# Kernel optimization log

Measured on AMD Instinct MI355X. Metric: run time of the kernel, lower is better.

Reference implementation:

```python
import jax, jax.numpy as jnp
import numpy as np

B, S, D = 2, 1024, 768
NH = 12
DH = D // NH
HID = 1536
G, EPG = 4, 2
E = G * EPG
TEMP = 1.0
LN_EPS = 1e-5


def setup_inputs() -> dict:
    key = jax.random.key(0)
    ks = jax.random.split(key, 8)
    s = 0.02
    return {
        "x": jax.random.normal(ks[0], (B, S, D), jnp.float32),
        "ln1_w": jnp.ones((D,), jnp.float32),
        "ln1_b": jnp.zeros((D,), jnp.float32),
        "in_proj_w": jax.random.normal(ks[1], (3 * D, D), jnp.float32) * s,
        "in_proj_b": jnp.zeros((3 * D,), jnp.float32),
        "out_proj_w": jax.random.normal(ks[2], (D, D), jnp.float32) * s,
        "out_proj_b": jnp.zeros((D,), jnp.float32),
        "ln2_w": jnp.ones((D,), jnp.float32),
        "ln2_b": jnp.zeros((D,), jnp.float32),
        "Wg": jax.random.normal(ks[3], (D, G), jnp.float32) * s,
        "bg": jnp.zeros((G,), jnp.float32),
        "We": jax.random.normal(ks[4], (G, D, EPG), jnp.float32) * s,
        "be": jnp.zeros((G, EPG), jnp.float32),
        "W1": jax.random.normal(ks[5], (E, D, HID), jnp.float32) * s,
        "b1": jnp.zeros((E, HID), jnp.float32),
        "W2": jax.random.normal(ks[6], (E, HID, D), jnp.float32) * s,
        "b2": jnp.zeros((E, D), jnp.float32),
    }


def _ln(x, w, b):
    m = x.mean(-1, keepdims=True)
    v = x.var(-1, keepdims=True)
    return (x - m) / jnp.sqrt(v + LN_EPS) * w + b


def _mha(h, wqkv, bqkv, wo, bo):
    qkv = h @ wqkv.T + bqkv                       # [B,S,3D]
    q, k, v = jnp.split(qkv, 3, axis=-1)
    q = q.reshape(B, S, NH, DH)
    k = k.reshape(B, S, NH, DH)
    v = v.reshape(B, S, NH, DH)
    scale = 1.0 / np.sqrt(DH).astype(np.float32)
    att = jnp.einsum("bqhd,bkhd->bhqk", q, k) * scale
    p = jax.nn.softmax(att, axis=-1)
    o = jnp.einsum("bhqk,bkhd->bqhd", p, v).reshape(B, S, D)
    return o @ wo.T + bo


def _moe(h, Wg, bg, We, be, W1, b1, W2, b2):
    hf = h.reshape(-1, D)                         # [N,D] tokens
    # level-1: group router (temperature softmax, top-1)
    gp = jax.nn.softmax((hf @ Wg + bg) / TEMP, axis=-1)          # [N,G]
    g = jnp.argmax(gp, axis=-1)                                   # [N]
    pg = jnp.take_along_axis(gp, g[:, None], axis=1)[:, 0]        # [N]
    # level-2: within-group expert router
    el = jnp.einsum("nd,gde->nge", hf, We) + be                   # [N,G,EPG]
    ep = jax.nn.softmax(el / TEMP, axis=-1)
    ep_g = jnp.take_along_axis(ep, g[:, None, None], axis=1)[:, 0, :]  # [N,EPG]
    e = jnp.argmax(ep_g, axis=-1)                                 # [N]
    pe = jnp.take_along_axis(ep_g, e[:, None], axis=1)[:, 0]      # [N]
    flat = g * EPG + e                                            # flat expert id [N]
    combine = jax.nn.one_hot(flat, E, dtype=hf.dtype) * (pg * pe)[:, None]  # [N,E]
    # dense expert compute (reference form of dispatch/grouped-GEMM/combine)
    hid = jax.nn.gelu(jnp.einsum("nd,edh->enh", hf, W1) + b1[:, None, :])   # [E,N,HID]
    y = jnp.einsum("enh,ehd->end", hid, W2) + b2[:, None, :]                # [E,N,D]
    out = jnp.einsum("ne,end->nd", combine, y)                              # [N,D]
    return out.reshape(h.shape)


def reference(x, ln1_w, ln1_b, in_proj_w, in_proj_b, out_proj_w, out_proj_b,
              ln2_w, ln2_b, Wg, bg, We, be, W1, b1, W2, b2):
    a = _mha(_ln(x, ln1_w, ln1_b), in_proj_w, in_proj_b, out_proj_w, out_proj_b)
    x = x + a  # dropout p=0.0 -> identity
    m = _moe(_ln(x, ln2_w, ln2_b), Wg, bg, We, be, W1, b1, W2, b2)
    return x + m
```

## Files before the change

kernel.cpp:

```cpp
#include <hip/hip_runtime.h>
#include <stdint.h>

#define B_ 2
#define S_ 1024
#define D_ 768
#define NH_ 12
#define DH_ 64
#define HID_ 1536
#define G_ 4
#define EPG_ 2
#define E_ 8
#define NTOK (B_*S_)
#define NGRP (B_*NH_*16)
#define KSPLIT 3

typedef unsigned short u16;
typedef unsigned int u32;
typedef __bf16 bf16x8 __attribute__((ext_vector_type(8)));
typedef float f32x4 __attribute__((ext_vector_type(4)));
typedef u16 u16x4 __attribute__((ext_vector_type(4)));
typedef u16 u16x8 __attribute__((ext_vector_type(8)));
typedef u32 u32x4 __attribute__((ext_vector_type(4)));

struct BfPair { u16 hi, lo; };

__device__ __forceinline__ u16 f2bf(float f){
  unsigned u = __builtin_bit_cast(unsigned, f);
  u += 0x7FFFu + ((u >> 16) & 1u);
  return (u16)(u >> 16);
}
__device__ __forceinline__ float bf2f(u16 h){
  unsigned u = ((unsigned)h) << 16;
  return __builtin_bit_cast(float, u);
}
__device__ __forceinline__ BfPair split_bf(float v){
  BfPair p;
  p.hi = f2bf(v);
  p.lo = f2bf(v - bf2f(p.hi));
  return p;
}
__device__ __forceinline__ float gelu_tanh(float x){
  float t = 0.7978845608028654f * (x + 0.044715f * x * x * x);
  float e = __expf(2.f * t);
  float th = 1.f - 2.f / (e + 1.f);
  return 0.5f * x * (1.f + th);
}
__device__ __forceinline__ void gload_lds16(const void* g, void* l){
  __builtin_amdgcn_global_load_lds(
      (const __attribute__((address_space(1))) void*)g,
      (__attribute__((address_space(3))) void*)l, 16, 0, 0);
}

__global__ __launch_bounds__(256) void k_prep(
    const float* __restrict__ in_proj_w, const float* __restrict__ out_proj_w,
    const float* __restrict__ W1, const float* __restrict__ W2,
    u16* __restrict__ inpTh, u16* __restrict__ inpTl,
    u16* __restrict__ outpTh, u16* __restrict__ outpTl,
    u16* __restrict__ W1t, u16* __restrict__ W2t){
  __shared__ float tile[32][33];
  int bid = blockIdx.x, t = threadIdx.x;
  if (bid < 2304){
    const float* src; u16 *dh, *dl; int i;
    if (bid < 1728){ src = in_proj_w; dh = inpTh; dl = inpTl; i = bid * 256 + t; }
    else           { src = out_proj_w; dh = outpTh; dl = outpTl; i = (bid - 1728) * 256 + t; }
    float4 v = ((const float4*)src)[i];
    u16x4 oh, ol;
    BfPair p0 = split_bf(v.x), p1 = split_bf(v.y), p2 = split_bf(v.z), p3 = split_bf(v.w);
    oh.x = p0.hi; ol.x = p0.lo; oh.y = p1.hi; ol.y = p1.lo;
    oh.z = p2.hi; ol.z = p2.lo; oh.w = p3.hi; ol.w = p3.lo;
    ((u16x4*)dh)[i] = oh;
    ((u16x4*)dl)[i] = ol;
  } else {
    const float* src; u16* dst; int R, C, cx, cy, e;
    if (bid < 11520){
      int r = bid - 2304; e = r / 1152; r %= 1152;
      R = D_; C = HID_; cx = r % 48; cy = r / 48;
      src = W1; dst = W1t;
    } else {
      int r = bid - 11520; e = r / 1152; r %= 1152;
      R = HID_; C = D_; cx = r % 24; cy = r / 24;
      src = W2; dst = W2t;
    }
    const float* s = src + (size_t)e * R * C;
    u16* d = dst + (size_t)e * R * C;
    int c0 = cx * 32, r0 = cy * 32;
    int tx = t & 31, ty = t >> 5;
    #pragma unroll
    for (int i = 0; i < 32; i += 8)
      tile[ty + i][tx] = s[(size_t)(r0 + ty + i) * C + c0 + tx];
    __syncthreads();
    #pragma unroll
    for (int i = 0; i < 32; i += 8)
      d[(size_t)(c0 + ty + i) * R + r0 + tx] = f2bf(tile[tx][ty + i]);
  }
}

template<int ROUTE>
__global__ __launch_bounds__(256) void k_layernorm(
    const float* __restrict__ x, const float* __restrict__ w, const float* __restrict__ b,
    u16* __restrict__ oh, u16* __restrict__ ol,
    const float* __restrict__ Wg, const float* __restrict__ bg,
    const float* __restrict__ We, const float* __restrict__ be,
    int* __restrict__ flat, float* __restrict__ pc){
  int row = blockIdx.x;
  const float* xr = x + (size_t)row * D_;
  int t = threadIdx.x;
  float v0 = xr[t], v1 = xr[t + 256], v2 = xr[t + 512];
  float s = v0 + v1 + v2;
  float sq = v0 * v0 + v1 * v1 + v2 * v2;
  #pragma unroll
  for (int m = 1; m < 64; m <<= 1){ s += __shfl_xor(s, m); sq += __shfl_xor(sq, m); }
  __shared__ float ls[4], lq[4];
  __shared__ float lred[4][4];
  int wid = t >> 6;
  if ((t & 63) == 0){ ls[wid] = s; lq[wid] = sq; }
  __syncthreads();
  s = ls[0] + ls[1] + ls[2] + ls[3];
  sq = lq[0] + lq[1] + lq[2] + lq[3];
  float mean = s * (1.f / D_);
  float var = sq * (1.f / D_) - mean * mean;
  float rstd = rsqrtf(var + 1e-5f);
  float y0, y1, y2;
  #pragma unroll
  for (int i = 0; i < 3; i++){
    int dcol = t + i * 256;
    float v = (i == 0 ? v0 : (i == 1 ? v1 : v2));
    float y = (v - mean) * rstd * w[dcol] + b[dcol];
    if (i == 0) y0 = y; else if (i == 1) y1 = y; else y2 = y;
    BfPair p = split_bf(y);
    oh[(size_t)row * D_ + dcol] = p.hi;
    if (ROUTE == 0) ol[(size_t)row * D_ + dcol] = p.lo;
  }
  if (ROUTE == 1){
    float gp[4] = {0.f, 0.f, 0.f, 0.f};
    #pragma unroll
    for (int i = 0; i < 3; i++){
      int dcol = t + i * 256;
      float y = (i == 0 ? y0 : (i == 1 ? y1 : y2));
      float4 wg = *(const float4*)&Wg[dcol * 4];
      gp[0] += y * wg.x; gp[1] += y * wg.y; gp[2] += y * wg.z; gp[3] += y * wg.w;
    }
    #pragma unroll
    for (int m = 1; m < 64; m <<= 1)
      #pragma unroll
      for (int j = 0; j < 4; j++) gp[j] += __shfl_xor(gp[j], m);
    if ((t & 63) == 0)
      #pragma unroll
      for (int j = 0; j < 4; j++) lred[wid][j] = gp[j];
    __syncthreads();
    float lg[4];
    #pragma unroll
    for (int j = 0; j < 4; j++)
      lg[j] = lred[0][j] + lred[1][j] + lred[2][j] + lred[3][j] + bg[j];
    int gi = 0; float gm = lg[0];
    #pragma unroll
    for (int j = 1; j < 4; j++) if (lg[j] > gm){ gm = lg[j]; gi = j; }
    float gs = 0.f;
    #pragma unroll
    for (int j = 0; j < 4; j++) gs += expf(lg[j] - gm);
    float pg = 1.f / gs;
    float e0 = 0.f, e1 = 0.f;
    #pragma unroll
    for (int i = 0; i < 3; i++){
      int dcol = t + i * 256;
      float y = (i == 0 ? y0 : (i == 1 ? y1 : y2));
      float2 we = *(const float2*)&We[((size_t)gi * D_ + dcol) * 2];
      e0 += y * we.x; e1 += y * we.y;
    }
    #pragma unroll
    for (int m = 1; m < 64; m <<= 1){ e0 += __shfl_xor(e0, m); e1 += __shfl_xor(e1, m); }
    __syncthreads();
    if ((t & 63) == 0){ lred[wid][0] = e0; lred[wid][1] = e1; }
    __syncthreads();
    if (t == 0){
      float E0 = lred[0][0] + lred[1][0] + lred[2][0] + lred[3][0] + be[gi * 2];
      float E1 = lred[0][1] + lred[1][1] + lred[2][1] + lred[3][1] + be[gi * 2 + 1];
      int ei; float pe;
      if (E1 > E0){ ei = 1; pe = 1.f / (1.f + expf(E0 - E1)); }
      else        { ei = 0; pe = 1.f / (1.f + expf(E1 - E0)); }
      flat[row] = gi * 2 + ei;
      pc[row] = pg * pe;
    }
  }
}

template<int EPI>
__global__ __launch_bounds__(256) void k_gemm3(
    const u16* __restrict__ Ah, const u16* __restrict__ Al,
    const u16* __restrict__ Bh, const u16* __restrict__ Bl,
    const float* __restrict__ bias, const float* __restrict__ resid,
    u16* __restrict__ outh, u16* __restrict__ outl, float* __restrict__ outf,
    u16* __restrict__ vth, u16* __restrict__ vtl,
    int M, int N, int K){
  __shared__ alignas(16) u16 Ash[2][128 * 32];
  __shared__ alignas(16) u16 Asl[2][128 * 32];
  __shared__ alignas(16) u16 Bsh[2][64 * 32];
  __shared__ alignas(16) u16 Bsl[2][64 * 32];
  int m0 = blockIdx.x * 128, n0 = blockIdx.y * 64;
  int tid = threadIdx.x, w = tid >> 6, l = tid & 63;
  f32x4 acc[2][4];
  #pragma unroll
  for (int i = 0; i < 2; i++)
    #pragma unroll
    for (int j = 0; j < 4; j++) acc[i][j] = f32x4{0.f, 0.f, 0.f, 0.f};
  int srow = l >> 2;
  int scol = 8 * ((l & 3) ^ ((l >> 2) & 3));
  const u16* gAh0 = Ah + (size_t)(m0 + w * 32 + srow) * K + scol;
  const u16* gAh1 = gAh0 + (size_t)16 * K;
  const u16* gAl0 = Al + (size_t)(m0 + w * 32 + srow) * K + scol;
  const u16* gAl1 = gAl0 + (size_t)16 * K;
  const u16* gBh = Bh + (size_t)(n0 + w * 16 + srow) * K + scol;
  const u16* gBl = Bl + (size_t)(n0 + w * 16 + srow) * K + scol;
  int dA0 = (w * 32) * 32, dA1 = (w * 32 + 16) * 32, dB = (w * 16) * 32;
  auto STAGE = [&](int buf, int k0){
    gload_lds16(gAh0 + k0, &Ash[buf][dA0]);
    gload_lds16(gAh1 + k0, &Ash[buf][dA1]);
    gload_lds16(gAl0 + k0, &Asl[buf][dA0]);
    gload_lds16(gAl1 + k0, &Asl[buf][dA1]);
    gload_lds16(gBh + k0, &Bsh[buf][dB]);
    gload_lds16(gBl + k0, &Bsl[buf][dB]);
  };
  STAGE(0, 0);
  __syncthreads();
  int nk = K / 32;
  int ca = (l >> 4) ^ (l & 3);
  int ai0 = (w * 32 + (l & 15)) * 32 + 8 * ca;
  int ai1 = ai0 + 16 * 32;
  for (int t = 0; t < nk; t++){
    int cur = t & 1;
    if (t + 1 < nk) STAGE(cur ^ 1, (t + 1) * 32);
    bf16x8 afh[2], afl[2], bfh[4], bfl[4];
    afh[0] = *(const bf16x8*)&Ash[cur][ai0];
    afh[1] = *(const bf16x8*)&Ash[cur][ai1];
    afl[0] = *(const bf16x8*)&Asl[cur][ai0];
    afl[1] = *(const bf16x8*)&Asl[cur][ai1];
    #pragma unroll
    for (int ni = 0; ni < 4; ni++){
      int bi = (ni * 16 + (l & 15)) * 32 + 8 * ca;
      bfh[ni] = *(const bf16x8*)&Bsh[cur][bi];
      bfl[ni] = *(const bf16x8*)&Bsl[cur][bi];
    }
    #pragma unroll
    for (int mi = 0; mi < 2; mi++)
      #pragma unroll
      for (int ni = 0; ni < 4; ni++){
        acc[mi][ni] = __builtin_amdgcn_mfma_f32_16x16x32_bf16(afh[mi], bfh[ni], acc[mi][ni], 0, 0, 0);
        acc[mi][ni] = __builtin_amdgcn_mfma_f32_16x16x32_bf16(afh[mi], bfl[ni], acc[mi][ni], 0, 0, 0);
        acc[mi][ni] = __builtin_amdgcn_mfma_f32_16x16x32_bf16(afl[mi], bfh[ni], acc[mi][ni], 0, 0, 0);
      }
    __syncthreads();
  }
  int r4 = (l >> 4) * 4, cc = l & 15;
  if (EPI == 0 && n0 >= 2 * D_){
    int hh = (n0 - 2 * D_) >> 6;
    int bb = m0 / S_;
    int bhl = bb * NH_ + hh;
    int sg0 = m0 % S_;
    u16* VhL = (u16*)&Ash[0][0];
    u16* VlL = (u16*)&Asl[0][0];
    #pragma unroll
    for (int mi = 0; mi < 2; mi++){
      #pragma unroll
      for (int ni = 0; ni < 4; ni++){
        int d = ni * 16 + cc;
        float bv = bias ? bias[n0 + d] : 0.f;
        int sl = w * 32 + mi * 16 + r4;
        u16x4 h4, l4;
        #pragma unroll
        for (int r = 0; r < 4; r++){
          BfPair p = split_bf(acc[mi][ni][r] + bv);
          h4[r] = p.hi; l4[r] = p.lo;
        }
        *(u16x4*)&VhL[d * 128 + sl] = h4;
        *(u16x4*)&VlL[d * 128 + sl] = l4;
      }
    }
    __syncthreads();
    for (int i = tid; i < 64 * 16; i += 256){
      int d = i >> 4, s8 = (i & 15) * 8;
      size_t go = ((size_t)bhl * DH_ + d) * S_ + sg0 + s8;
      *(u16x8*)&vth[go] = *(const u16x8*)&VhL[d * 128 + s8];
      *(u16x8*)&vtl[go] = *(const u16x8*)&VlL[d * 128 + s8];
    }
    return;
  }
  #pragma unroll
  for (int mi = 0; mi < 2; mi++){
    #pragma unroll
    for (int ni = 0; ni < 4; ni++){
      int col = n0 + ni * 16 + cc;
      float bv = bias ? bias[col] : 0.f;
      #pragma unroll
      for (int r = 0; r < 4; r++){
        int row = m0 + w * 32 + mi * 16 + r4 + r;
        float v = acc[mi][ni][r] + bv;
        if (EPI == 0){
          BfPair p = split_bf(v);
          outh[(size_t)row * N + col] = p.hi;
          outl[(size_t)row * N + col] = p.lo;
        } else {
          outf[(size_t)row * N + col] = v + resid[(size_t)row * N + col];
        }
      }
    }
  }
}

__global__ __launch_bounds__(256) void k_attn3(
    const u16* __restrict__ qkvh, const u16* __restrict__ qkvl,
    const u16* __restrict__ vth, const u16* __restrict__ vtl,
    float* __restrict__ po0, float* __restrict__ po1, float* __restrict__ po2,
    float* __restrict__ pm, float* __restrict__ plsum){
  __shared__ alignas(16) u16 Ksh[2][32 * 64];
  __shared__ alignas(16) u16 Ksl[2][32 * 64];
  __shared__ alignas(16) u16 Vsh[2][64 * 32];
  __shared__ alignas(16) u16 Vsl[2][64 * 32];
  int bh = blockIdx.x, qb = blockIdx.y, ks = blockIdx.z;
  int b = bh / NH_, h = bh % NH_;
  int g = bh * 16 + qb;
  int tid = threadIdx.x, w = tid >> 6, l = tid & 63;
  int q0 = qb * 64 + w * 16;
  const int RS = 3 * D_;
  size_t qoff = (size_t)(b * S_ + q0 + (l & 15)) * RS + h * DH_ + 8 * (l >> 4);
  bf16x8 aqh[2], aql[2];
  aqh[0] = *(const bf16x8*)(qkvh + qoff); aqh[1] = *(const bf16x8*)(qkvh + qoff + 32);
  aql[0] = *(const bf16x8*)(qkvl + qoff); aql[1] = *(const bf16x8*)(qkvl + qoff + 32);
  f32x4 oacc[4];
  #pragma unroll
  for (int i = 0; i < 4; i++) oacc[i] = f32x4{0.f, 0.f, 0.f, 0.f};
  float mrun = -1e30f, lrun = 0.f;

  size_t koff = (size_t)(b * S_ + w * 8 + (l >> 3)) * RS + D_ + h * DH_ + 8 * ((l & 7) ^ (l >> 3));
  const u16* Kgh = qkvh + koff;
  const u16* Kgl = qkvl + koff;
  size_t voff = ((size_t)bh * DH_ + w * 16 + (l >> 2)) * S_ + 8 * ((l & 3) ^ ((l >> 2) & 3));
  const u16* Vgh = vth + voff;
  const u16* Vgl = vtl + voff;
  int wdst = w * 512;

  auto STAGE = [&](int buf, int akt){
    gload_lds16(Kgh + (size_t)(akt * 32) * RS, &Ksh[buf][wdst]);
    gload_lds16(Kgl + (size_t)(akt * 32) * RS, &Ksl[buf][wdst]);
    gload_lds16(Vgh + akt * 32, &Vsh[buf][wdst]);
    gload_lds16(Vgl + akt * 32, &Vsl[buf][wdst]);
  };
  int kt0 = (ks * 32) / KSPLIT;
  int ktE = ((ks + 1) * 32) / KSPLIT;
  STAGE(0, kt0);
  __syncthreads();

  int ck0 = (l >> 4) ^ (l & 7);
  int ck1 = ck0 ^ 4;
  int cv = (l >> 4) ^ (l & 3);
  int s1 = (l & 15) | ((l & 16) << 1);
  int s2 = s1 + 16;
  bool up = (l & 32) != 0;

  for (int kt = kt0; kt < ktE; kt++){
    int cur = (kt - kt0) & 1;
    if (kt + 1 < ktE) STAGE(cur ^ 1, kt + 1);
    f32x4 st[2];
    #pragma unroll
    for (int nt = 0; nt < 2; nt++){
      int rbase = (nt * 16 + (l & 15)) * 64;
      bf16x8 kh0 = *(const bf16x8*)&Ksh[cur][rbase + 8 * ck0];
      bf16x8 kh1 = *(const bf16x8*)&Ksh[cur][rbase + 8 * ck1];
      bf16x8 kl0 = *(const bf16x8*)&Ksl[cur][rbase + 8 * ck0];
      bf16x8 kl1 = *(const bf16x8*)&Ksl[cur][rbase + 8 * ck1];
      f32x4 c = f32x4{0.f, 0.f, 0.f, 0.f};
      c = __builtin_amdgcn_mfma_f32_16x16x32_bf16(kh0, aqh[0], c, 0, 0, 0);
      c = __builtin_amdgcn_mfma_f32_16x16x32_bf16(kh1, aqh[1], c, 0, 0, 0);
      c = __builtin_amdgcn_mfma_f32_16x16x32_bf16(kh0, aql[0], c, 0, 0, 0);
      c = __builtin_amdgcn_mfma_f32_16x16x32_bf16(kh1, aql[1], c, 0, 0, 0);
      c = __builtin_amdgcn_mfma_f32_16x16x32_bf16(kl0, aqh[0], c, 0, 0, 0);
      c = __builtin_amdgcn_mfma_f32_16x16x32_bf16(kl1, aqh[1], c, 0, 0, 0);
      st[nt] = c;
    }
    float mx = fmaxf(fmaxf(fmaxf(st[0][0], st[0][1]), fmaxf(st[0][2], st[0][3])),
                     fmaxf(fmaxf(st[1][0], st[1][1]), fmaxf(st[1][2], st[1][3])));
    mx = fmaxf(mx, __shfl_xor(mx, 16));
    mx = fmaxf(mx, __shfl_xor(mx, 32));
    mx *= 0.125f;
    if (!__all(mx <= mrun)){
      float mnew = fmaxf(mrun, mx);
      float alpha = __expf(mrun - mnew);
      lrun *= alpha;
      #pragma unroll
      for (int r = 0; r < 4; r++){
        float ar = __shfl(alpha, (l & 48) | (((l >> 4) << 2) + r));
        oacc[0][r] *= ar; oacc[1][r] *= ar; oacc[2][r] *= ar; oacc[3][r] *= ar;
      }
      mrun = mnew;
    }
    float p[8]; float sum = 0.f;
    #pragma unroll
    for (int j = 0; j < 8; j++){
      p[j] = __expf(st[j >> 2][j & 3] * 0.125f - mrun);
      sum += p[j];
    }
    sum += __shfl_xor(sum, 16);
    sum += __shfl_xor(sum, 32);
    lrun += sum;
    u32 pkh[4], pkl[4];
    #pragma unroll
    for (int i = 0; i < 4; i++){
      BfPair a = split_bf(p[2 * i]), bb = split_bf(p[2 * i + 1]);
      pkh[i] = (u32)a.hi | ((u32)bb.hi << 16);
      pkl[i] = (u32)a.lo | ((u32)bb.lo << 16);
    }
    u32 ah0 = __shfl((int)pkh[0], s1), ah1 = __shfl((int)pkh[1], s1);
    u32 ah2 = __shfl((int)pkh[2], s1), ah3 = __shfl((int)pkh[3], s1);
    u32 bh0 = __shfl((int)pkh[0], s2), bh1 = __shfl((int)pkh[1], s2);
    u32 bh2 = __shfl((int)pkh[2], s2), bh3 = __shfl((int)pkh[3], s2);
    u32 al0 = __shfl((int)pkl[0], s1), al1 = __shfl((int)pkl[1], s1);
    u32 al2 = __shfl((int)pkl[2], s1), al3 = __shfl((int)pkl[3], s1);
    u32 bl0 = __shfl((int)pkl[0], s2), bl1 = __shfl((int)pkl[1], s2);
    u32 bl2 = __shfl((int)pkl[2], s2), bl3 = __shfl((int)pkl[3], s2);
    u32x4 fh, fl;
    fh.x = up ? ah2 : ah0; fh.y = up ? ah3 : ah1; fh.z = up ? bh2 : bh0; fh.w = up ? bh3 : bh1;
    fl.x = up ? al2 : al0; fl.y = up ? al3 : al1; fl.z = up ? bl2 : bl0; fl.w = up ? bl3 : bl1;
    bf16x8 pa_h = __builtin_bit_cast(bf16x8, fh);
    bf16x8 pa_l = __builtin_bit_cast(bf16x8, fl);
    #pragma unroll
    for (int dt = 0; dt < 4; dt++){
      int vb = (dt * 16 + (l & 15)) * 32 + 8 * cv;
      bf16x8 bvh = *(const bf16x8*)&Vsh[cur][vb];
      bf16x8 bvl = *(const bf16x8*)&Vsl[cur][vb];
      oacc[dt] = __builtin_amdgcn_mfma_f32_16x16x32_bf16(pa_h, bvh, oacc[dt], 0, 0, 0);
      oacc[dt] = __builtin_amdgcn_mfma_f32_16x16x32_bf16(pa_h, bvl, oacc[dt], 0, 0, 0);
      oacc[dt] = __builtin_amdgcn_mfma_f32_16x16x32_bf16(pa_l, bvh, oacc[dt], 0, 0, 0);
    }
    __syncthreads();
  }
  float* po = (ks == 0) ? po0 : ((ks == 1) ? po1 : po2);
  #pragma unroll
  for (int dt = 0; dt < 4; dt++)
    #pragma unroll
    for (int r = 0; r < 4; r++){
      int qloc = w * 16 + (l >> 4) * 4 + r;
      int d = dt * 16 + (l & 15);
      po[((size_t)(g * 64 + qloc)) * 64 + d] = oacc[dt][r];
    }
  if (l < 16){
    pm[(ks * NGRP + g) * 64 + w * 16 + l] = mrun;
    plsum[(ks * NGRP + g) * 64 + w * 16 + l] = lrun;
  }
}

__global__ __launch_bounds__(256) void k_attn_merge(
    const float* __restrict__ po0, const float* __restrict__ po1, const float* __restrict__ po2,
    const float* __restrict__ pm, const float* __restrict__ plsum,
    u16* __restrict__ oh, u16* __restrict__ ol){
  int bh = blockIdx.x, qb = blockIdx.y;
  int b = bh / NH_, h = bh % NH_;
  int g = bh * 16 + qb;
  int t = threadIdx.x;
  int q = t >> 2, d0 = (t & 3) * 16;
  float m0 = pm[g * 64 + q];
  float m1 = pm[(NGRP + g) * 64 + q];
  float m2 = pm[(2 * NGRP + g) * 64 + q];
  float l0 = plsum[g * 64 + q];
  float l1 = plsum[(NGRP + g) * 64 + q];
  float l2 = plsum[(2 * NGRP + g) * 64 + q];
  float M = fmaxf(fmaxf(m0, m1), m2);
  float a0 = __expf(m0 - M), a1 = __expf(m1 - M), a2 = __expf(m2 - M);
  float rcp = 1.f / (l0 * a0 + l1 * a1 + l2 * a2);
  size_t base = ((size_t)(g * 64 + q)) * 64 + d0;
  size_t orow = (size_t)(b * S_ + qb * 64 + q) * D_ + h * DH_ + d0;
  #pragma unroll
  for (int j = 0; j < 16; j++){
    float v = (po0[base + j] * a0 + po1[base + j] * a1 + po2[base + j] * a2) * rcp;
    BfPair p = split_bf(v);
    oh[orow + j] = p.hi;
    ol[orow + j] = p.lo;
  }
}

__global__ __launch_bounds__(1024) void k_bucket(
    const int* __restrict__ flat, int* __restrict__ moeI, int* __restrict__ order){
  __shared__ int cnt[E_], off[E_], cur[E_];
  int t = threadIdx.x;
  if (t < E_){ cnt[t] = 0; cur[t] = 0; }
  __syncthreads();
  int n0 = t, n1 = t + 1024;
  int f0 = flat[n0], f1 = flat[n1];
  atomicAdd(&cnt[f0], 1);
  atomicAdd(&cnt[f1], 1);
  __syncthreads();
  if (t == 0){
    int s = 0;
    for (int e = 0; e < E_; e++){
      off[e] = s; moeI[16 + e] = s; moeI[e] = cnt[e]; s += cnt[e];
    }
  }
  __syncthreads();
  int p0 = atomicAdd(&cur[f0], 1);
  order[off[f0] + p0] = n0;
  int p1 = atomicAdd(&cur[f1], 1);
  order[off[f1] + p1] = n1;
}

__global__ __launch_bounds__(256) void k_moe_gemm1(
    const u16* __restrict__ h2, const u16* __restrict__ W1t, const float* __restrict__ b1,
    const int* __restrict__ order, const int* __restrict__ moeI, u16* __restrict__ hid){
  int e = blockIdx.x, mt = blockIdx.y, nt = blockIdx.z;
  int cnt = moeI[e];
  if (mt * 64 >= cnt) return;
  int off = moeI[16 + e];
  __shared__ alignas(16) u16 As[2][64 * 64];
  __shared__ alignas(16) u16 Bs[2][64 * 64];
  int tid = threadIdx.x, w = tid >> 6, l = tid & 63;
  int wr = w >> 1, wc = w & 1;
  f32x4 acc[2][2];
  #pragma unroll
  for (int i = 0; i < 2; i++)
    #pragma unroll
    for (int j = 0; j < 2; j++) acc[i][j] = f32x4{0.f, 0.f, 0.f, 0.f};
  int r0 = w * 16 + (l >> 3);
  int sch = 8 * ((l & 7) ^ (l >> 3));
  int tokA0 = order[off + min(mt * 64 + r0, cnt - 1)];
  int tokA1 = order[off + min(mt * 64 + r0 + 8, cnt - 1)];
  const u16* gA0 = h2 + (size_t)tokA0 * D_ + sch;
  const u16* gA1 = h2 + (size_t)tokA1 * D_ + sch;
  const u16* gB0 = W1t + (size_t)e * HID_ * D_ + (size_t)(nt * 64 + r0) * D_ + sch;
  const u16* gB1 = gB0 + (size_t)8 * D_;
  int d0 = (w * 16) * 64, d1 = (w * 16 + 8) * 64;
  auto STAGE = [&](int buf, int k0){
    gload_lds16(gA0 + k0, &As[buf][d0]);
    gload_lds16(gA1 + k0, &As[buf][d1]);
    gload_lds16(gB0 + k0, &Bs[buf][d0]);
    gload_lds16(gB1 + k0, &Bs[buf][d1]);
  };
  STAGE(0, 0);
  __syncthreads();
  int c0 = (l >> 4) ^ (l & 7);
  int c1 = ((l >> 4) + 4) ^ (l & 7);
  const int nk = D_ / 64;
  for (int t = 0; t < nk; t++){
    int cur = t & 1;
    if (t + 1 < nk) STAGE(cur ^ 1, (t + 1) * 64);
    bf16x8 af[2][2], bfr[2][2];
    #pragma unroll
    for (int mi = 0; mi < 2; mi++){
      int rbase = (wr * 32 + mi * 16 + (l & 15)) * 64;
      af[mi][0] = *(const bf16x8*)&As[cur][rbase + 8 * c0];
      af[mi][1] = *(const bf16x8*)&As[cur][rbase + 8 * c1];
    }
    #pragma unroll
    for (int ni = 0; ni < 2; ni++){
      int rbase = (wc * 32 + ni * 16 + (l & 15)) * 64;
      bfr[ni][0] = *(const bf16x8*)&Bs[cur][rbase + 8 * c0];
      bfr[ni][1] = *(const bf16x8*)&Bs[cur][rbase + 8 * c1];
    }
    #pragma unroll
    for (int mi = 0; mi < 2; mi++)
      #pragma unroll
      for (int ni = 0; ni < 2; ni++){
        acc[mi][ni] = __builtin_amdgcn_mfma_f32_16x16x32_bf16(af[mi][0], bfr[ni][0], acc[mi][ni], 0, 0, 0);
        acc[mi][ni] = __builtin_amdgcn_mfma_f32_16x16x32_bf16(af[mi][1], bfr[ni][1], acc[mi][ni], 0, 0, 0);
      }
    __syncthreads();
  }
  int r4 = (l >> 4) * 4, cc = l & 15;
  #pragma unroll
  for (int mi = 0; mi < 2; mi++){
    #pragma unroll
    for (int ni = 0; ni < 2; ni++){
      int col = nt * 64 + wc * 32 + ni * 16 + cc;
      float bv = b1[e * HID_ + col];
      #pragma unroll
      for (int r = 0; r < 4; r++){
        int rowl = mt * 64 + wr * 32 + mi * 16 + r4 + r;
        if (rowl < cnt){
          float v = gelu_tanh(acc[mi][ni][r] + bv);
          hid[(size_t)(off + rowl) * HID_ + col] = f2bf(v);
        }
      }
    }
  }
}

__global__ __launch_bounds__(256) void k_moe_gemm2(
    const u16* __restrict__ hid, const u16* __restrict__ W2t, const float* __restrict__ b2,
    const int* __restrict__ order, const int* __restrict__ moeI,
    const float* __restrict__ pc, const float* __restrict__ x2, float* __restrict__ out){
  int e = blockIdx.x, mt = blockIdx.y, nt = blockIdx.z;
  int cnt = moeI[e];
  if (mt * 64 >= cnt) return;
  int off = moeI[16 + e];
  __shared__ alignas(16) u16 As[2][64 * 64];
  __shared__ alignas(16) u16 Bs[2][64 * 64];
  int tid = threadIdx.x, w = tid >> 6, l = tid & 63;
  int wr = w >> 1, wc = w & 1;
  f32x4 acc[2][2];
  #pragma unroll
  for (int i = 0; i < 2; i++)
    #pragma unroll
    for (int j = 0; j < 2; j++) acc[i][j] = f32x4{0.f, 0.f, 0.f, 0.f};
  int r0 = w * 16 + (l >> 3);
  int sch = 8 * ((l & 7) ^ (l >> 3));
  int ar0 = off + min(mt * 64 + r0, cnt - 1);
  int ar1 = off + min(mt * 64 + r0 + 8, cnt - 1);
  const u16* gA0 = hid + (size_t)ar0 * HID_ + sch;
  const u16* gA1 = hid + (size_t)ar1 * HID_ + sch;
  const u16* gB0 = W2t + (size_t)e * D_ * HID_ + (size_t)(nt * 64 + r0) * HID_ + sch;
  const u16* gB1 = gB0 + (size_t)8 * HID_;
  int d0 = (w * 16) * 64, d1 = (w * 16 + 8) * 64;
  auto STAGE = [&](int buf, int k0){
    gload_lds16(gA0 + k0, &As[buf][d0]);
    gload_lds16(gA1 + k0, &As[buf][d1]);
    gload_lds16(gB0 + k0, &Bs[buf][d0]);
    gload_lds16(gB1 + k0, &Bs[buf][d1]);
  };
  STAGE(0, 0);
  __syncthreads();
  int c0 = (l >> 4) ^ (l & 7);
  int c1 = ((l >> 4) + 4) ^ (l & 7);
  const int nk = HID_ / 64;
  for (int t = 0; t < nk; t++){
    int cur = t & 1;
    if (t + 1 < nk) STAGE(cur ^ 1, (t + 1) * 64);
    bf16x8 af[2][2], bfr[2][2];
    #pragma unroll
    for (int mi = 0; mi < 2; mi++){
      int rbase = (wr * 32 + mi * 16 + (l & 15)) * 64;
      af[mi][0] = *(const bf16x8*)&As[cur][rbase + 8 * c0];
      af[mi][1] = *(const bf16x8*)&As[cur][rbase + 8 * c1];
    }
    #pragma unroll
    for (int ni = 0; ni < 2; ni++){
      int rbase = (wc * 32 + ni * 16 + (l & 15)) * 64;
      bfr[ni][0] = *(const bf16x8*)&Bs[cur][rbase + 8 * c0];
      bfr[ni][1] = *(const bf16x8*)&Bs[cur][rbase + 8 * c1];
    }
    #pragma unroll
    for (int mi = 0; mi < 2; mi++)
      #pragma unroll
      for (int ni = 0; ni < 2; ni++){
        acc[mi][ni] = __builtin_amdgcn_mfma_f32_16x16x32_bf16(af[mi][0], bfr[ni][0], acc[mi][ni], 0, 0, 0);
        acc[mi][ni] = __builtin_amdgcn_mfma_f32_16x16x32_bf16(af[mi][1], bfr[ni][1], acc[mi][ni], 0, 0, 0);
      }
    __syncthreads();
  }
  int r4 = (l >> 4) * 4, cc = l & 15;
  #pragma unroll
  for (int mi = 0; mi < 2; mi++){
    #pragma unroll
    for (int r = 0; r < 4; r++){
      int rowl = mt * 64 + wr * 32 + mi * 16 + r4 + r;
      if (rowl < cnt){
        int tok = order[off + rowl];
        float pv = pc[tok];
        #pragma unroll
        for (int ni = 0; ni < 2; ni++){
          int col = nt * 64 + wc * 32 + ni * 16 + cc;
          float v = acc[mi][ni][r] + b2[e * D_ + col];
          out[(size_t)tok * D_ + col] = x2[(size_t)tok * D_ + col] + pv * v;
        }
      }
    }
  }
}

extern "C" void kernel_launch(void* const* d_in, const int* in_sizes, int n_in,
                              void* d_out, int out_size, void* d_ws, size_t ws_size,
                              hipStream_t stream){
  const float* x         = (const float*)d_in[0];
  const float* ln1_w     = (const float*)d_in[1];
  const float* ln1_b     = (const float*)d_in[2];
  const float* in_proj_w = (const float*)d_in[3];
  const float* in_proj_b = (const float*)d_in[4];
  const float* out_proj_w= (const float*)d_in[5];
  const float* out_proj_b= (const float*)d_in[6];
  const float* ln2_w     = (const float*)d_in[7];
  const float* ln2_b     = (const float*)d_in[8];
  const float* Wg        = (const float*)d_in[9];
  const float* bg        = (const float*)d_in[10];
  const float* We        = (const float*)d_in[11];
  const float* be        = (const float*)d_in[12];
  const float* W1        = (const float*)d_in[13];
  const float* b1        = (const float*)d_in[14];
  const float* W2        = (const float*)d_in[15];
  const float* b2        = (const float*)d_in[16];
  float* out = (float*)d_out;

  char* ws = (char*)d_ws;
  size_t off = 0;
  auto alloc = [&](size_t bytes) -> char* {
    char* p = ws + off;
    off += (bytes + 255) & ~(size_t)255;
    return p;
  };
  u16*   inpTh = (u16*)  alloc((size_t)3 * D_ * D_ * 2);
  u16*   inpTl = (u16*)  alloc((size_t)3 * D_ * D_ * 2);
  u16*   outpTh= (u16*)  alloc((size_t)D_ * D_ * 2);
  u16*   outpTl= (u16*)  alloc((size_t)D_ * D_ * 2);
  u16*   W1t  = (u16*)  alloc((size_t)E_ * HID_ * D_ * 2);
  u16*   W2t  = (u16*)  alloc((size_t)E_ * D_ * HID_ * 2);
  u16*   qkvh = (u16*)  alloc((size_t)NTOK * 3 * D_ * 2);
  u16*   qkvl = (u16*)  alloc((size_t)NTOK * 3 * D_ * 2);
  u16*   h1h  = (u16*)  alloc((size_t)NTOK * D_ * 2);
  u16*   h1l  = (u16*)  alloc((size_t)NTOK * D_ * 2);
  u16*   vth  = (u16*)  alloc((size_t)B_ * NH_ * DH_ * S_ * 2);
  u16*   vtl  = (u16*)  alloc((size_t)B_ * NH_ * DH_ * S_ * 2);
  float* x2   = (float*)alloc((size_t)NTOK * D_ * 4);
  u16*   h2   = (u16*)  alloc((size_t)NTOK * D_ * 2);
  int*   flat = (int*)  alloc(NTOK * 4);
  float* pc   = (float*)alloc(NTOK * 4);
  int*   order= (int*)  alloc(NTOK * 4);
  int*   moeI = (int*)  alloc(32 * 4);
  float* po0  = (float*)h1h;
  float* po1  = (float*)inpTh;
  float* po2  = x2;
  float* pmArr= (float*)((char*)inpTh + 6291456);
  float* plArr= (float*)((char*)inpTh + 6291456 + 294912);
  u16*   attnh= qkvh;
  u16*   attnl= qkvl;
  u16*   hid  = (u16*)qkvl;

  k_prep<<<dim3(20736), dim3(256), 0, stream>>>(
      in_proj_w, out_proj_w, W1, W2, inpTh, inpTl, outpTh, outpTl, W1t, W2t);
  k_layernorm<0><<<dim3(NTOK), dim3(256), 0, stream>>>(
      x, ln1_w, ln1_b, h1h, h1l, nullptr, nullptr, nullptr, nullptr, nullptr, nullptr);
  k_gemm3<0><<<dim3(NTOK / 128, 3 * D_ / 64), dim3(256), 0, stream>>>(
      h1h, h1l, inpTh, inpTl, in_proj_b, nullptr, qkvh, qkvl, nullptr, vth, vtl, NTOK, 3 * D_, D_);
  k_attn3<<<dim3(B_ * NH_, S_ / 64, KSPLIT), dim3(256), 0, stream>>>(
      qkvh, qkvl, vth, vtl, po0, po1, po2, pmArr, plArr);
  k_attn_merge<<<dim3(B_ * NH_, S_ / 64), dim3(256), 0, stream>>>(
      po0, po1, po2, pmArr, plArr, attnh, attnl);
  k_gemm3<1><<<dim3(NTOK / 128, D_ / 64), dim3(256), 0, stream>>>(
      attnh, attnl, outpTh, outpTl, out_proj_b, x, nullptr, nullptr, x2,
      (u16*)nullptr, (u16*)nullptr, NTOK, D_, D_);
  k_layernorm<1><<<dim3(NTOK), dim3(256), 0, stream>>>(
      x2, ln2_w, ln2_b, h2, nullptr, Wg, bg, We, be, flat, pc);
  k_bucket<<<dim3(1), dim3(1024), 0, stream>>>(flat, moeI, order);
  k_moe_gemm1<<<dim3(E_, NTOK / 64, HID_ / 64), dim3(256), 0, stream>>>(h2, W1t, b1, order, moeI, hid);
  k_moe_gemm2<<<dim3(E_, NTOK / 64, D_ / 64), dim3(256), 0, stream>>>(hid, W2t, b2, order, moeI, pc, x2, out);
}
```

Before: 200.0 us.

## Double attention query tile to 128 rows with 8 waves sharing K/V staging

The attention kernel now uses 512 threads per block covering 128 query rows, so each staged K/V tile in LDS is reused by twice as many query waves. Staging is split across waves: the first four load K and the last four load V. The intent is to halve global K/V traffic and staging instructions per query. In exchange there are fewer blocks, which lowers occupancy and parallelism on the GPU, and the larger barrier groups add synchronization cost. Output indexing is rewritten to stay compatible with the existing merge kernel layout.

```diff
diff --git a/kernel.cpp b/kernel.cpp
--- a/kernel.cpp
+++ b/kernel.cpp
@@ -306,7 +306,7 @@
   }
 }
 
-__global__ __launch_bounds__(256) void k_attn3(
+__global__ __launch_bounds__(512) void k_attn3(
     const u16* __restrict__ qkvh, const u16* __restrict__ qkvl,
     const u16* __restrict__ vth, const u16* __restrict__ vtl,
     float* __restrict__ po0, float* __restrict__ po1, float* __restrict__ po2,
@@ -317,9 +317,8 @@
   __shared__ alignas(16) u16 Vsl[2][64 * 32];
   int bh = blockIdx.x, qb = blockIdx.y, ks = blockIdx.z;
   int b = bh / NH_, h = bh % NH_;
-  int g = bh * 16 + qb;
   int tid = threadIdx.x, w = tid >> 6, l = tid & 63;
-  int q0 = qb * 64 + w * 16;
+  int q0 = qb * 128 + w * 16;
   const int RS = 3 * D_;
   size_t qoff = (size_t)(b * S_ + q0 + (l & 15)) * RS + h * DH_ + 8 * (l >> 4);
   bf16x8 aqh[2], aql[2];
@@ -330,19 +329,26 @@
   for (int i = 0; i < 4; i++) oacc[i] = f32x4{0.f, 0.f, 0.f, 0.f};
   float mrun = -1e30f, lrun = 0.f;
 
-  size_t koff = (size_t)(b * S_ + w * 8 + (l >> 3)) * RS + D_ + h * DH_ + 8 * ((l & 7) ^ (l >> 3));
-  const u16* Kgh = qkvh + koff;
-  const u16* Kgl = qkvl + koff;
-  size_t voff = ((size_t)bh * DH_ + w * 16 + (l >> 2)) * S_ + 8 * ((l & 3) ^ ((l >> 2) & 3));
-  const u16* Vgh = vth + voff;
-  const u16* Vgl = vtl + voff;
-  int wdst = w * 512;
-
+  const u16 *Sg0, *Sg1;
+  u16 *Sd0h, *Sd0l, *Sd1h, *Sd1l;
+  size_t sstep;
+  if (w < 4){
+    size_t koff = (size_t)(b * S_ + w * 8 + (l >> 3)) * RS + D_ + h * DH_ + 8 * ((l & 7) ^ (l >> 3));
+    Sg0 = qkvh + koff; Sg1 = qkvl + koff;
+    Sd0h = &Ksh[0][w * 512]; Sd0l = &Ksl[0][w * 512];
+    Sd1h = &Ksh[1][w * 512]; Sd1l = &Ksl[1][w * 512];
+    sstep = 0;
+  } else {
+    size_t voff = ((size_t)bh * DH_ + (w - 4) * 16 + (l >> 2)) * S_ + 8 * ((l & 3) ^ ((l >> 2) & 3));
+    Sg0 = vth + voff; Sg1 = vtl + voff;
+    Sd0h = &Vsh[0][(w - 4) * 512]; Sd0l = &Vsl[0][(w - 4) * 512];
+    Sd1h = &Vsh[1][(w - 4) * 512]; Sd1l = &Vsl[1][(w - 4) * 512];
+    sstep = 1;
+  }
   auto STAGE = [&](int buf, int akt){
-    gload_lds16(Kgh + (size_t)(akt * 32) * RS, &Ksh[buf][wdst]);
-    gload_lds16(Kgl + (size_t)(akt * 32) * RS, &Ksl[buf][wdst]);
-    gload_lds16(Vgh + akt * 32, &Vsh[buf][wdst]);
-    gload_lds16(Vgl + akt * 32, &Vsl[buf][wdst]);
+    size_t off = (sstep == 0) ? (size_t)(akt * 32) * RS : (size_t)(akt * 32);
+    gload_lds16(Sg0 + off, buf ? Sd1h : Sd0h);
+    gload_lds16(Sg1 + off, buf ? Sd1l : Sd0l);
   };
   int kt0 = (ks * 32) / KSPLIT;
   int ktE = ((ks + 1) * 32) / KSPLIT;
@@ -437,13 +443,14 @@
   for (int dt = 0; dt < 4; dt++)
     #pragma unroll
     for (int r = 0; r < 4; r++){
-      int qloc = w * 16 + (l >> 4) * 4 + r;
+      int qg = qb * 128 + w * 16 + (l >> 4) * 4 + r;
       int d = dt * 16 + (l & 15);
-      po[((size_t)(g * 64 + qloc)) * 64 + d] = oacc[dt][r];
+      po[((size_t)(bh * 1024 + qg)) * 64 + d] = oacc[dt][r];
     }
   if (l < 16){
-    pm[(ks * NGRP + g) * 64 + w * 16 + l] = mrun;
-    plsum[(ks * NGRP + g) * 64 + w * 16 + l] = lrun;
+    int qg = qb * 128 + w * 16 + l;
+    pm[ks * (NGRP * 64) + bh * 1024 + qg] = mrun;
+    plsum[ks * (NGRP * 64) + bh * 1024 + qg] = lrun;
   }
 }
 
@@ -724,7 +731,7 @@
       x, ln1_w, ln1_b, h1h, h1l, nullptr, nullptr, nullptr, nullptr, nullptr, nullptr);
   k_gemm3<0><<<dim3(NTOK / 128, 3 * D_ / 64), dim3(256), 0, stream>>>(
       h1h, h1l, inpTh, inpTl, in_proj_b, nullptr, qkvh, qkvl, nullptr, vth, vtl, NTOK, 3 * D_, D_);
-  k_attn3<<<dim3(B_ * NH_, S_ / 64, KSPLIT), dim3(256), 0, stream>>>(
+  k_attn3<<<dim3(B_ * NH_, S_ / 128, KSPLIT), dim3(512), 0, stream>>>(
       qkvh, qkvl, vth, vtl, po0, po1, po2, pmArr, plArr);
   k_attn_merge<<<dim3(B_ * NH_, S_ / 64), dim3(256), 0, stream>>>(
       po0, po1, po2, pmArr, plArr, attnh, attnl);
```

Result: no change. 203.5 us (+1.8%).
